# Kernel optimization log

Hardware: AMD Instinct MI355X
Metric: run time of the kernel (lower is better)

## Reference

```python
import jax, jax.numpy as jnp
import numpy as np

ATT_HEAD, IN_DIM, OUT_DIM = 8, 768, 96
B, N = 8, 1024
LEAKY_ALPHA = 0.2


def setup_inputs() -> dict:
    key = jax.random.key(0)
    ks = jax.random.split(key, 8)
    feat_in = jax.random.normal(ks[0], (B, N, IN_DIM), dtype=jnp.float32)
    adj = jax.random.randint(ks[1], (B, N, N), 0, 2).astype(jnp.float32)
    # xavier-ish init scales
    W = jax.random.normal(ks[2], (ATT_HEAD, IN_DIM, OUT_DIM), dtype=jnp.float32) * (1.0 / np.sqrt(IN_DIM))
    b = jnp.zeros((OUT_DIM,), dtype=jnp.float32)
    w_src = jax.random.normal(ks[3], (ATT_HEAD, OUT_DIM, 1), dtype=jnp.float32) * (1.0 / np.sqrt(OUT_DIM))
    w_dst = jax.random.normal(ks[4], (ATT_HEAD, OUT_DIM, 1), dtype=jnp.float32) * (1.0 / np.sqrt(OUT_DIM))
    Hw = jax.random.normal(ks[5], (IN_DIM, IN_DIM), dtype=jnp.float32) * (1.0 / np.sqrt(IN_DIM))
    Hb = jnp.zeros((IN_DIM,), dtype=jnp.float32)
    return {"feat_in": feat_in, "adj": adj, "W": W, "b": b,
            "w_src": w_src, "w_dst": w_dst, "Hw": Hw, "Hb": Hb}


def reference(feat_in, adj, W, b, w_src, w_dst, Hw, Hb):
    batch, n, _ = feat_in.shape
    # per-head projection: [B,H,N,O]
    h = jnp.einsum('bni,hio->bhno', feat_in, W)
    t = jnp.tanh(h)
    a_src = jnp.einsum('bhno,hoq->bhnq', t, w_src)[..., 0]  # [B,H,N]
    a_dst = jnp.einsum('bhno,hoq->bhnq', t, w_dst)[..., 0]  # [B,H,N]
    attn = a_src[:, :, :, None] + a_dst[:, :, None, :]       # [B,H,N,N]
    attn = jnp.where(attn >= 0, attn, LEAKY_ALPHA * attn)
    mask = adj[:, None, :, :] == 0                            # 1-adj as bool
    attn = jnp.where(mask, jnp.float32(-999.0), attn)
    attn = jax.nn.softmax(attn, axis=-1)
    feat_out = jnp.einsum('bhnm,bhmo->bhno', attn, h) + b     # [B,H,N,O]
    feat_out = jnp.transpose(feat_out, (0, 2, 1, 3)).reshape(batch, n, -1)
    feat_out = jax.nn.elu(feat_out)
    gate = jax.nn.sigmoid(feat_in @ Hw.T + Hb)
    return gate * feat_out + (1.0 - gate) * feat_in
```

## Files before the change

### kernel.cpp

```cpp
#include <hip/hip_runtime.h>
#include <cstddef>

#define BATCH 8
#define NN 1024
#define IN_DIM 768
#define OUT_DIM 96
#define HEADS 8
#define M_ROWS 8192
#define NCOLS 1536

typedef __attribute__((ext_vector_type(8))) short short8;
typedef __attribute__((ext_vector_type(4))) float f32x4;
typedef __attribute__((ext_vector_type(4))) unsigned short ushort4v;

typedef __attribute__((address_space(1))) void gvoid_t;
typedef __attribute__((address_space(3))) void lvoid_t;

__device__ __forceinline__ void gload_lds16(const void* g, void* l) {
    __builtin_amdgcn_global_load_lds((gvoid_t*)(unsigned long long)g,
                                     (lvoid_t*)(unsigned int)(unsigned long long)l,
                                     16, 0, 0);
}

__device__ __forceinline__ unsigned short f2bf(float x) {
    unsigned int u = __builtin_bit_cast(unsigned int, x);
    u += 0x7fffu + ((u >> 16) & 1u);
    return (unsigned short)(u >> 16);
}
__device__ __forceinline__ float bf2f(unsigned short u) {
    unsigned int v = ((unsigned int)u) << 16;
    return __builtin_bit_cast(float, v);
}
__device__ __forceinline__ float tanh_fast(float x) {
    return 1.f - 2.f / (__expf(2.f * x) + 1.f);
}

__global__ void xb_kernel(const float* __restrict__ x, unsigned short* __restrict__ xb) {
    int idx = blockIdx.x * 256 + threadIdx.x;
    const float4* p = (const float4*)(x + (size_t)idx * 8);
    float4 a = p[0], b = p[1];
    short8 r;
    r[0] = (short)f2bf(a.x); r[1] = (short)f2bf(a.y); r[2] = (short)f2bf(a.z); r[3] = (short)f2bf(a.w);
    r[4] = (short)f2bf(b.x); r[5] = (short)f2bf(b.y); r[6] = (short)f2bf(b.z); r[7] = (short)f2bf(b.w);
    *(short8*)(xb + (size_t)idx * 8) = r;
}

__global__ void pack_w_kernel(const float* __restrict__ W, unsigned short* __restrict__ BT) {
    int idx = blockIdx.x * 256 + threadIdx.x;
    int c = idx / IN_DIM, i = idx % IN_DIM;
    int h = c / OUT_DIM, o = c % OUT_DIM;
    BT[(size_t)c * IN_DIM + i] = f2bf(W[((size_t)h * IN_DIM + i) * OUT_DIM + o]);
}
__global__ void pack_hw_kernel(const float* __restrict__ Hw, unsigned short* __restrict__ BT) {
    int idx = blockIdx.x * 256 + threadIdx.x;
    int c = idx / IN_DIM, i = idx % IN_DIM;
    BT[(size_t)(768 + c) * IN_DIM + i] = f2bf(Hw[(size_t)c * IN_DIM + i]);
}

__global__ void pack_abits_kernel(const float* __restrict__ adj, unsigned int* __restrict__ abits) {
    int idx = blockIdx.x * 256 + threadIdx.x;
    const float4* p = (const float4*)(adj + (size_t)idx * 32);
    unsigned int m = 0;
    #pragma unroll
    for (int q = 0; q < 8; ++q) {
        float4 v = p[q];
        m |= (v.x != 0.f ? 1u : 0u) << (q * 4 + 0);
        m |= (v.y != 0.f ? 1u : 0u) << (q * 4 + 1);
        m |= (v.z != 0.f ? 1u : 0u) << (q * 4 + 2);
        m |= (v.w != 0.f ? 1u : 0u) << (q * 4 + 3);
    }
    abits[idx] = m;
}

__global__ __launch_bounds__(256) void gemm1_kernel(
        const unsigned short* __restrict__ Xb, const unsigned short* __restrict__ BT,
        const float* __restrict__ Hb,
        unsigned short* __restrict__ h_bt, unsigned short* __restrict__ gate) {
    __shared__ __align__(16) unsigned short As[128 * 64];
    __shared__ __align__(16) unsigned short Bs[128 * 64];
    __shared__ float hbs[128];
    int m0 = blockIdx.x * 128;
    int c0 = blockIdx.y * 128;
    int t = threadIdx.x;
    int w = t >> 6, lane = t & 63, l15 = t & 15, quad = lane >> 4;
    if (c0 >= 768 && t < 128) hbs[t] = Hb[c0 - 768 + t];
    f32x4 acc[2][8] = {};
    for (int k0 = 0; k0 < IN_DIM; k0 += 64) {
        __syncthreads();
        #pragma unroll
        for (int cc = 0; cc < 4; ++cc) {
            int base64 = (w * 4 + cc) * 64;
            int p = base64 + lane;
            int r = p >> 3, qs = p & 7;
            int qb = qs ^ (r & 7);
            gload_lds16(Xb + (size_t)(m0 + r) * IN_DIM + k0 + qb * 8, As + base64 * 8);
            gload_lds16(BT + (size_t)(c0 + r) * IN_DIM + k0 + qb * 8, Bs + base64 * 8);
        }
        __syncthreads();
        #pragma unroll
        for (int ks = 0; ks < 2; ++ks) {
            short8 af[2], bfr[8];
            #pragma unroll
            for (int mt = 0; mt < 2; ++mt) {
                int r = w * 32 + mt * 16 + l15;
                int cb = (ks * 4 + quad) ^ (r & 7);
                af[mt] = *(const short8*)(As + r * 64 + cb * 8);
            }
            #pragma unroll
            for (int nt = 0; nt < 8; ++nt) {
                int r = nt * 16 + l15;
                int cb = (ks * 4 + quad) ^ (r & 7);
                bfr[nt] = *(const short8*)(Bs + r * 64 + cb * 8);
            }
            #pragma unroll
            for (int mt = 0; mt < 2; ++mt)
                #pragma unroll
                for (int nt = 0; nt < 8; ++nt)
                    acc[mt][nt] = __builtin_amdgcn_mfma_f32_16x16x32_bf16(af[mt], bfr[nt], acc[mt][nt], 0, 0, 0);
        }
    }
    int b = m0 >> 10;
    #pragma unroll
    for (int mt = 0; mt < 2; ++mt) {
        int rowbase = m0 + w * 32 + mt * 16 + quad * 4;
        int nbase = rowbase & 1023;
        #pragma unroll
        for (int nt = 0; nt < 8; ++nt) {
            int c = c0 + nt * 16 + l15;
            if (c < 768) {
                int hh = c / OUT_DIM, o = c % OUT_DIM;
                ushort4v hb;
                hb[0] = f2bf(acc[mt][nt][0]); hb[1] = f2bf(acc[mt][nt][1]);
                hb[2] = f2bf(acc[mt][nt][2]); hb[3] = f2bf(acc[mt][nt][3]);
                *(ushort4v*)(h_bt + ((size_t)(b * 8 + hh) * OUT_DIM + o) * NN + nbase) = hb;
            } else {
                int cl = nt * 16 + l15;
                int cg = c - 768;
                #pragma unroll
                for (int reg = 0; reg < 4; ++reg) {
                    float z = acc[mt][nt][reg] + hbs[cl];
                    float g = __builtin_amdgcn_rcpf(1.f + __builtin_amdgcn_exp2f(-1.44269504f * z));
                    _Float16 gh = (_Float16)g;
                    gate[(size_t)(rowbase + reg) * 768 + cg] = __builtin_bit_cast(unsigned short, gh);
                }
            }
        }
    }
}

__global__ __launch_bounds__(256) void a_kernel(const unsigned short* __restrict__ h_bt,
                                                const float* __restrict__ w_src,
                                                const float* __restrict__ w_dst,
                                                float* __restrict__ a_src, float* __restrict__ a_dst) {
    __shared__ unsigned short ht[96 * 72];
    __shared__ float ws_s[96], wd_s[96];
    __shared__ float pps[4][64], ppd[4][64];
    int bh = blockIdx.x >> 4;
    int n0 = (blockIdx.x & 15) * 64;
    int head = bh & 7;
    int t = threadIdx.x;
    if (t < 96) { ws_s[t] = w_src[head * 96 + t]; wd_s[t] = w_dst[head * 96 + t]; }
    for (int f = t; f < 768; f += 256) {
        int row = f >> 3, c8 = (f & 7) * 8;
        *(short8*)(ht + row * 72 + c8) = *(const short8*)(h_bt + ((size_t)bh * 96 + row) * NN + n0 + c8);
    }
    __syncthreads();
    int n = t & 63, part = t >> 6;
    float ps = 0.f, pd = 0.f;
    #pragma unroll
    for (int oo = 0; oo < 24; ++oo) {
        int o = part * 24 + oo;
        float th = tanh_fast(bf2f(ht[o * 72 + n]));
        ps += th * ws_s[o];
        pd += th * wd_s[o];
    }
    pps[part][n] = ps; ppd[part][n] = pd;
    __syncthreads();
    if (t < 64) {
        float s = pps[0][t] + pps[1][t] + pps[2][t] + pps[3][t];
        float d = ppd[0][t] + ppd[1][t] + ppd[2][t] + ppd[3][t];
        a_src[bh * 1024 + n0 + t] = s * 1.44269504f;
        a_dst[bh * 1024 + n0 + t] = d * 1.44269504f;
    }
}

__global__ __launch_bounds__(512) void attn_kernel(
        const unsigned short* __restrict__ h_bt, const unsigned int* __restrict__ abits,
        const float* __restrict__ a_src_g, const float* __restrict__ a_dst_g,
        const unsigned short* __restrict__ gate, const unsigned short* __restrict__ Xb,
        const float* __restrict__ bias, float* __restrict__ out) {
    __shared__ __align__(16) unsigned short hs[2][96 * 64];
    __shared__ __align__(16) float adst[1024];
    __shared__ float bias_s[96];
    int blk = blockIdx.x;
    int bh = blk >> 3, i0 = (blk & 7) * 128, b = bh >> 3, hh = bh & 7;
    int t = threadIdx.x;
    int w = t >> 6, lane = t & 63, l15 = t & 15, quad = lane >> 4;
    if (t < 256) *(f32x4*)(adst + t * 4) = *(const f32x4*)(a_dst_g + bh * 1024 + t * 4);
    if (t < 96) bias_s[t] = bias[t];
    int irow = i0 + w * 16 + l15;
    float si = a_src_g[bh * 1024 + irow];
    const unsigned short* hhp = h_bt + (size_t)bh * 96 * NN;
    if (w < 6) {
        #pragma unroll
        for (int cc = 0; cc < 2; ++cc) {
            int u0 = (w * 2 + cc) * 64;
            int p = u0 + lane;
            int r = p >> 3, qs = p & 7, qb = qs ^ (r & 7);
            gload_lds16(hhp + (size_t)r * NN + qb * 8, (char*)&hs[0][0] + (size_t)u0 * 16);
        }
    }
    const unsigned int* mrow = abits + ((size_t)b * NN + irow) * 32;
    uint2 mw = *(const uint2*)(mrow);
    f32x4 acc[7] = {};
    short8 ones = {};
    if (l15 == 0) {
        #pragma unroll
        for (int u = 0; u < 8; ++u) ones[u] = (short)0x3F80;
    }
    __syncthreads();
    for (int j0 = 0; j0 < 1024; j0 += 64) {
        int cur = (j0 >> 6) & 1;
        int jn = j0 + 64;
        if (jn < 1024 && w < 6) {
            #pragma unroll
            for (int cc = 0; cc < 2; ++cc) {
                int u0 = (w * 2 + cc) * 64;
                int p = u0 + lane;
                int r = p >> 3, qs = p & 7, qb = qs ^ (r & 7);
                gload_lds16(hhp + (size_t)r * NN + jn + qb * 8, (char*)&hs[cur ^ 1][0] + (size_t)u0 * 16);
            }
        }
        short8 af[2];
        unsigned int mws[2] = {mw.x, mw.y};
        #pragma unroll
        for (int ks = 0; ks < 2; ++ks) {
            unsigned int byte = (mws[ks] >> (quad * 8)) & 0xFFu;
            f32x4 d0 = *(const f32x4*)(&adst[j0 + ks * 32 + quad * 8]);
            f32x4 d1 = *(const f32x4*)(&adst[j0 + ks * 32 + quad * 8 + 4]);
            float dv[8] = {d0[0], d0[1], d0[2], d0[3], d1[0], d1[1], d1[2], d1[3]};
            float ev[8];
            #pragma unroll
            for (int u = 0; u < 8; ++u) {
                float s = si + dv[u];
                float l = fmaxf(s, 0.2f * s);
                float e = __builtin_amdgcn_exp2f(l);
                ev[u] = ((byte >> u) & 1u) ? e : 0.f;
            }
            union { unsigned int u4[4]; short8 s8; } pk;
            #pragma unroll
            for (int p2 = 0; p2 < 4; ++p2) {
                unsigned int u0b = __builtin_bit_cast(unsigned int, ev[2 * p2]) + 0x8000u;
                unsigned int u1b = __builtin_bit_cast(unsigned int, ev[2 * p2 + 1]) + 0x8000u;
                pk.u4[p2] = __builtin_amdgcn_perm(u1b, u0b, 0x07060302);
            }
            af[ks] = pk.s8;
        }
        if (jn < 1024) mw = *(const uint2*)(mrow + (jn >> 5));
        #pragma unroll
        for (int ks = 0; ks < 2; ++ks) {
            #pragma unroll
            for (int nt = 0; nt < 6; ++nt) {
                int r = nt * 16 + l15;
                int qs = (ks * 4 + quad) ^ (r & 7);
                short8 bfr = *(const short8*)(&hs[cur][(size_t)(r * 8 + qs) * 8]);
                acc[nt] = __builtin_amdgcn_mfma_f32_16x16x32_bf16(af[ks], bfr, acc[nt], 0, 0, 0);
            }
            acc[6] = __builtin_amdgcn_mfma_f32_16x16x32_bf16(af[ks], ones, acc[6], 0, 0, 0);
        }
        __syncthreads();
    }
    int rowq = i0 + w * 16 + quad * 4;
    #pragma unroll
    for (int reg = 0; reg < 4; ++reg) {
        float ssum = __shfl(acc[6][reg], (lane & 48));
        float inv = (ssum > 0.f) ? __builtin_amdgcn_rcpf(ssum) : 0.f;
        int n = rowq + reg;
        size_t mrow_o = ((size_t)b * NN + n) * 768 + hh * 96;
        #pragma unroll
        for (int nt = 0; nt < 6; ++nt) {
            int cl = nt * 16 + l15;
            float v = acc[nt][reg] * inv + bias_s[cl];
            float e = (v > 0.f) ? v : (__builtin_amdgcn_exp2f(v * 1.44269504f) - 1.f);
            _Float16 gh = __builtin_bit_cast(_Float16, gate[mrow_o + cl]);
            float g = (float)gh;
            float x = bf2f(Xb[mrow_o + cl]);
            out[mrow_o + cl] = x + g * (e - x);
        }
    }
}

extern "C" void kernel_launch(void* const* d_in, const int* in_sizes, int n_in,
                              void* d_out, int out_size, void* d_ws, size_t ws_size,
                              hipStream_t stream) {
    const float* feat_in = (const float*)d_in[0];
    const float* adj     = (const float*)d_in[1];
    const float* W       = (const float*)d_in[2];
    const float* bbias   = (const float*)d_in[3];
    const float* w_src   = (const float*)d_in[4];
    const float* w_dst   = (const float*)d_in[5];
    const float* Hw      = (const float*)d_in[6];
    const float* Hb      = (const float*)d_in[7];
    float* out = (float*)d_out;
    char* base = (char*)d_ws;

    unsigned short* Xb    = (unsigned short*)(base);
    unsigned short* BcatT = (unsigned short*)(base + 12582912);
    unsigned short* h_bt  = (unsigned short*)(base + 14942208);
    unsigned short* gate  = (unsigned short*)(base + 27525120);
    float* a_src = (float*)(base + 40108032);
    float* a_dst = (float*)(base + 40370176);
    unsigned int* abits = (unsigned int*)(base + 40632320);

    xb_kernel<<<(M_ROWS * IN_DIM / 8) / 256, 256, 0, stream>>>(feat_in, Xb);
    pack_w_kernel<<<(768 * IN_DIM) / 256, 256, 0, stream>>>(W, BcatT);
    pack_hw_kernel<<<(768 * IN_DIM) / 256, 256, 0, stream>>>(Hw, BcatT);
    pack_abits_kernel<<<(BATCH * NN * NN / 32) / 256, 256, 0, stream>>>(adj, abits);
    gemm1_kernel<<<dim3(M_ROWS / 128, NCOLS / 128), 256, 0, stream>>>(Xb, BcatT, Hb, h_bt, gate);
    a_kernel<<<64 * 16, 256, 0, stream>>>(h_bt, w_src, w_dst, a_src, a_dst);
    attn_kernel<<<64 * 8, 512, 0, stream>>>(h_bt, abits, a_src, a_dst, gate, Xb, bbias, out);
}
```

Baseline: 190.9 us.

## Switch bf16 to fp16 with packed conversions and merge prep kernels into one launch

All intermediate operands (inputs, weights, h, attention probabilities) now use fp16 instead of bf16. MFMA calls become the f16 variant, and conversions use the hardware packed round-toward-zero instruction in place of manual bit-twiddling. The four preprocessing kernels are merged into a single launch that dispatches on block index, which removes launch overhead and tail gaps between them. The exponent range of fp16 is narrower than bf16, so large projection values or unnormalized exp values could overflow. Round-toward-zero also adds a small bias.

```diff
diff --git a/kernel.cpp b/kernel.cpp
--- a/kernel.cpp
+++ b/kernel.cpp
@@ -12,6 +12,7 @@
 typedef __attribute__((ext_vector_type(8))) short short8;
 typedef __attribute__((ext_vector_type(4))) float f32x4;
 typedef __attribute__((ext_vector_type(4))) unsigned short ushort4v;
+typedef _Float16 half8 __attribute__((ext_vector_type(8)));
 
 typedef __attribute__((address_space(1))) void gvoid_t;
 typedef __attribute__((address_space(3))) void lvoid_t;
@@ -22,54 +23,64 @@
                                      16, 0, 0);
 }
 
-__device__ __forceinline__ unsigned short f2bf(float x) {
-    unsigned int u = __builtin_bit_cast(unsigned int, x);
-    u += 0x7fffu + ((u >> 16) & 1u);
-    return (unsigned short)(u >> 16);
-}
-__device__ __forceinline__ float bf2f(unsigned short u) {
-    unsigned int v = ((unsigned int)u) << 16;
-    return __builtin_bit_cast(float, v);
+__device__ __forceinline__ unsigned int pkrtz(float a, float b) {
+    return __builtin_bit_cast(unsigned int, __builtin_amdgcn_cvt_pkrtz(a, b));
+}
+__device__ __forceinline__ unsigned short f2h(float x) {
+    _Float16 h = (_Float16)x;
+    return __builtin_bit_cast(unsigned short, h);
+}
+__device__ __forceinline__ float h2f(unsigned short u) {
+    return (float)__builtin_bit_cast(_Float16, u);
 }
 __device__ __forceinline__ float tanh_fast(float x) {
     return 1.f - 2.f / (__expf(2.f * x) + 1.f);
 }
-
-__global__ void xb_kernel(const float* __restrict__ x, unsigned short* __restrict__ xb) {
-    int idx = blockIdx.x * 256 + threadIdx.x;
-    const float4* p = (const float4*)(x + (size_t)idx * 8);
-    float4 a = p[0], b = p[1];
-    short8 r;
-    r[0] = (short)f2bf(a.x); r[1] = (short)f2bf(a.y); r[2] = (short)f2bf(a.z); r[3] = (short)f2bf(a.w);
-    r[4] = (short)f2bf(b.x); r[5] = (short)f2bf(b.y); r[6] = (short)f2bf(b.z); r[7] = (short)f2bf(b.w);
-    *(short8*)(xb + (size_t)idx * 8) = r;
-}
-
-__global__ void pack_w_kernel(const float* __restrict__ W, unsigned short* __restrict__ BT) {
-    int idx = blockIdx.x * 256 + threadIdx.x;
-    int c = idx / IN_DIM, i = idx % IN_DIM;
-    int h = c / OUT_DIM, o = c % OUT_DIM;
-    BT[(size_t)c * IN_DIM + i] = f2bf(W[((size_t)h * IN_DIM + i) * OUT_DIM + o]);
-}
-__global__ void pack_hw_kernel(const float* __restrict__ Hw, unsigned short* __restrict__ BT) {
-    int idx = blockIdx.x * 256 + threadIdx.x;
-    int c = idx / IN_DIM, i = idx % IN_DIM;
-    BT[(size_t)(768 + c) * IN_DIM + i] = f2bf(Hw[(size_t)c * IN_DIM + i]);
-}
-
-__global__ void pack_abits_kernel(const float* __restrict__ adj, unsigned int* __restrict__ abits) {
-    int idx = blockIdx.x * 256 + threadIdx.x;
-    const float4* p = (const float4*)(adj + (size_t)idx * 32);
-    unsigned int m = 0;
-    #pragma unroll
-    for (int q = 0; q < 8; ++q) {
-        float4 v = p[q];
-        m |= (v.x != 0.f ? 1u : 0u) << (q * 4 + 0);
-        m |= (v.y != 0.f ? 1u : 0u) << (q * 4 + 1);
-        m |= (v.z != 0.f ? 1u : 0u) << (q * 4 + 2);
-        m |= (v.w != 0.f ? 1u : 0u) << (q * 4 + 3);
-    }
-    abits[idx] = m;
+__device__ __forceinline__ f32x4 mfma16(short8 a, short8 b, f32x4 c) {
+    return __builtin_amdgcn_mfma_f32_16x16x32_f16(
+        __builtin_bit_cast(half8, a), __builtin_bit_cast(half8, b), c, 0, 0, 0);
+}
+
+__global__ __launch_bounds__(256) void prep_kernel(
+        const float* __restrict__ feat_in, const float* __restrict__ W,
+        const float* __restrict__ Hw, const float* __restrict__ adj,
+        unsigned short* __restrict__ Xb, unsigned short* __restrict__ BT,
+        unsigned int* __restrict__ abits) {
+    int blk = blockIdx.x;
+    int t = threadIdx.x;
+    if (blk < 3072) {
+        int idx = blk * 256 + t;
+        const float4* p = (const float4*)(feat_in + (size_t)idx * 8);
+        float4 a = p[0], b = p[1];
+        union { unsigned int u4[4]; short8 s8; } pk;
+        pk.u4[0] = pkrtz(a.x, a.y);
+        pk.u4[1] = pkrtz(a.z, a.w);
+        pk.u4[2] = pkrtz(b.x, b.y);
+        pk.u4[3] = pkrtz(b.z, b.w);
+        *(short8*)(Xb + (size_t)idx * 8) = pk.s8;
+    } else if (blk < 5376) {
+        int idx = (blk - 3072) * 256 + t;
+        int c = idx / IN_DIM, i = idx % IN_DIM;
+        int h = c / OUT_DIM, o = c % OUT_DIM;
+        BT[(size_t)c * IN_DIM + i] = f2h(W[((size_t)h * IN_DIM + i) * OUT_DIM + o]);
+    } else if (blk < 7680) {
+        int idx = (blk - 5376) * 256 + t;
+        int c = idx / IN_DIM, i = idx % IN_DIM;
+        BT[(size_t)(768 + c) * IN_DIM + i] = f2h(Hw[(size_t)c * IN_DIM + i]);
+    } else {
+        int idx = (blk - 7680) * 256 + t;
+        const float4* p = (const float4*)(adj + (size_t)idx * 32);
+        unsigned int m = 0;
+        #pragma unroll
+        for (int q = 0; q < 8; ++q) {
+            float4 v = p[q];
+            m |= (v.x != 0.f ? 1u : 0u) << (q * 4 + 0);
+            m |= (v.y != 0.f ? 1u : 0u) << (q * 4 + 1);
+            m |= (v.z != 0.f ? 1u : 0u) << (q * 4 + 2);
+            m |= (v.w != 0.f ? 1u : 0u) << (q * 4 + 3);
+        }
+        abits[idx] = m;
+    }
 }
 
 __global__ __launch_bounds__(256) void gemm1_kernel(
@@ -116,7 +127,7 @@
             for (int mt = 0; mt < 2; ++mt)
                 #pragma unroll
                 for (int nt = 0; nt < 8; ++nt)
-                    acc[mt][nt] = __builtin_amdgcn_mfma_f32_16x16x32_bf16(af[mt], bfr[nt], acc[mt][nt], 0, 0, 0);
+                    acc[mt][nt] = mfma16(af[mt], bfr[nt], acc[mt][nt]);
         }
     }
     int b = m0 >> 10;
@@ -129,10 +140,10 @@
             int c = c0 + nt * 16 + l15;
             if (c < 768) {
                 int hh = c / OUT_DIM, o = c % OUT_DIM;
-                ushort4v hb;
-                hb[0] = f2bf(acc[mt][nt][0]); hb[1] = f2bf(acc[mt][nt][1]);
-                hb[2] = f2bf(acc[mt][nt][2]); hb[3] = f2bf(acc[mt][nt][3]);
-                *(ushort4v*)(h_bt + ((size_t)(b * 8 + hh) * OUT_DIM + o) * NN + nbase) = hb;
+                union { unsigned int u2[2]; ushort4v u4; } pk;
+                pk.u2[0] = pkrtz(acc[mt][nt][0], acc[mt][nt][1]);
+                pk.u2[1] = pkrtz(acc[mt][nt][2], acc[mt][nt][3]);
+                *(ushort4v*)(h_bt + ((size_t)(b * 8 + hh) * OUT_DIM + o) * NN + nbase) = pk.u4;
             } else {
                 int cl = nt * 16 + l15;
                 int cg = c - 768;
@@ -140,8 +151,7 @@
                 for (int reg = 0; reg < 4; ++reg) {
                     float z = acc[mt][nt][reg] + hbs[cl];
                     float g = __builtin_amdgcn_rcpf(1.f + __builtin_amdgcn_exp2f(-1.44269504f * z));
-                    _Float16 gh = (_Float16)g;
-                    gate[(size_t)(rowbase + reg) * 768 + cg] = __builtin_bit_cast(unsigned short, gh);
+                    gate[(size_t)(rowbase + reg) * 768 + cg] = f2h(g);
                 }
             }
         }
@@ -170,7 +180,7 @@
     #pragma unroll
     for (int oo = 0; oo < 24; ++oo) {
         int o = part * 24 + oo;
-        float th = tanh_fast(bf2f(ht[o * 72 + n]));
+        float th = tanh_fast(h2f(ht[o * 72 + n]));
         ps += th * ws_s[o];
         pd += th * wd_s[o];
     }
@@ -216,7 +226,7 @@
     short8 ones = {};
     if (l15 == 0) {
         #pragma unroll
-        for (int u = 0; u < 8; ++u) ones[u] = (short)0x3F80;
+        for (int u = 0; u < 8; ++u) ones[u] = (short)0x3C00;
     }
     __syncthreads();
     for (int j0 = 0; j0 < 1024; j0 += 64) {
@@ -248,12 +258,10 @@
                 ev[u] = ((byte >> u) & 1u) ? e : 0.f;
             }
             union { unsigned int u4[4]; short8 s8; } pk;
-            #pragma unroll
-            for (int p2 = 0; p2 < 4; ++p2) {
-                unsigned int u0b = __builtin_bit_cast(unsigned int, ev[2 * p2]) + 0x8000u;
-                unsigned int u1b = __builtin_bit_cast(unsigned int, ev[2 * p2 + 1]) + 0x8000u;
-                pk.u4[p2] = __builtin_amdgcn_perm(u1b, u0b, 0x07060302);
-            }
+            pk.u4[0] = pkrtz(ev[0], ev[1]);
+            pk.u4[1] = pkrtz(ev[2], ev[3]);
+            pk.u4[2] = pkrtz(ev[4], ev[5]);
+            pk.u4[3] = pkrtz(ev[6], ev[7]);
             af[ks] = pk.s8;
         }
         if (jn < 1024) mw = *(const uint2*)(mrow + (jn >> 5));
@@ -264,9 +272,9 @@
                 int r = nt * 16 + l15;
                 int qs = (ks * 4 + quad) ^ (r & 7);
                 short8 bfr = *(const short8*)(&hs[cur][(size_t)(r * 8 + qs) * 8]);
-                acc[nt] = __builtin_amdgcn_mfma_f32_16x16x32_bf16(af[ks], bfr, acc[nt], 0, 0, 0);
-            }
-            acc[6] = __builtin_amdgcn_mfma_f32_16x16x32_bf16(af[ks], ones, acc[6], 0, 0, 0);
+                acc[nt] = mfma16(af[ks], bfr, acc[nt]);
+            }
+            acc[6] = mfma16(af[ks], ones, acc[6]);
         }
         __syncthreads();
     }
@@ -282,9 +290,8 @@
             int cl = nt * 16 + l15;
             float v = acc[nt][reg] * inv + bias_s[cl];
             float e = (v > 0.f) ? v : (__builtin_amdgcn_exp2f(v * 1.44269504f) - 1.f);
-            _Float16 gh = __builtin_bit_cast(_Float16, gate[mrow_o + cl]);
-            float g = (float)gh;
-            float x = bf2f(Xb[mrow_o + cl]);
+            float g = h2f(gate[mrow_o + cl]);
+            float x = h2f(Xb[mrow_o + cl]);
             out[mrow_o + cl] = x + g * (e - x);
         }
     }
@@ -312,10 +319,7 @@
     float* a_dst = (float*)(base + 40370176);
     unsigned int* abits = (unsigned int*)(base + 40632320);
 
-    xb_kernel<<<(M_ROWS * IN_DIM / 8) / 256, 256, 0, stream>>>(feat_in, Xb);
-    pack_w_kernel<<<(768 * IN_DIM) / 256, 256, 0, stream>>>(W, BcatT);
-    pack_hw_kernel<<<(768 * IN_DIM) / 256, 256, 0, stream>>>(Hw, BcatT);
-    pack_abits_kernel<<<(BATCH * NN * NN / 32) / 256, 256, 0, stream>>>(adj, abits);
+    prep_kernel<<<8704, 256, 0, stream>>>(feat_in, W, Hw, adj, Xb, BcatT, abits);
     gemm1_kernel<<<dim3(M_ROWS / 128, NCOLS / 128), 256, 0, stream>>>(Xb, BcatT, Hb, h_bt, gate);
     a_kernel<<<64 * 16, 256, 0, stream>>>(h_bt, w_src, w_dst, a_src, a_dst);
     attn_kernel<<<64 * 8, 512, 0, stream>>>(h_bt, abits, a_src, a_dst, gate, Xb, bbias, out);
```

New measurement: 187.7 us. No clear change (-1.7%).
